# Optimization experiments

Measured on AMD Instinct MI355X. Metric: run time of the kernel, lower is better.

Reference implementation:

```python
import jax, jax.numpy as jnp
import numpy as np

D_MODEL = 1024
NUM_HEADS = 16
D_K = D_MODEL // NUM_HEADS
B, S = 4, 2048


def setup_inputs() -> dict:
    key = jax.random.key(0)
    k1, k2, k3 = jax.random.split(key, 3)
    x = jax.random.normal(k1, (B, S, D_MODEL), dtype=jnp.float32)
    w_qkv = jax.random.normal(k2, (3, NUM_HEADS, D_K, D_MODEL), dtype=jnp.float32) / np.sqrt(D_MODEL)
    w_o = jax.random.normal(k3, (D_MODEL, D_MODEL), dtype=jnp.float32) / np.sqrt(D_MODEL)
    return {"x": x, "w_qkv": w_qkv, "w_o": w_o}


def reference(x, w_qkv, w_o):
    # x: [b, s, m]; w_qkv: [3, h, k, m]; w_o: [m, m]
    seq_len = x.shape[-2]
    d_k = w_qkv.shape[-2]
    # fused QKV projection for all heads: [3, b, h, s, k]
    qkv = jnp.einsum('bsm,qhkm->qbhsk', x, w_qkv)
    Q, K, V = qkv[0], qkv[1], qkv[2]
    # attention scores [b, h, s, s]
    scores = jnp.einsum('bhsk,bhtk->bhst', Q, K) / jnp.sqrt(jnp.asarray(d_k, x.dtype))
    # causal mask: position t > s is masked
    causal = jnp.tril(jnp.ones((seq_len, seq_len), dtype=bool))
    scores = jnp.where(causal, scores, -jnp.inf)
    probs = jax.nn.softmax(scores, axis=-1)
    # attn_pdrop = 0.0 -> dropout is identity
    attn = jnp.einsum('bhst,bhtk->bhsk', probs, V)
    # concat heads: [b, s, h*k]
    b, h, s, k = attn.shape
    attn_cat = jnp.transpose(attn, (0, 2, 1, 3)).reshape(b, s, h * k)
    # output projection: y = attn_cat @ w_o^T
    return jnp.einsum('bsd,md->bsm', attn_cat, w_o)
```

## Files before the change

### kernel.cpp

```cpp
#include <hip/hip_runtime.h>
#include <hip/hip_bf16.h>


#define D_MODEL 1024
#define NUM_HEADS 16
#define D_KD 64
#define B_SZ 4
#define S_LEN 2048
#define ROWS (B_SZ * S_LEN)
#define QKV_N (3 * D_MODEL)

typedef __attribute__((ext_vector_type(8))) short short8;
typedef __attribute__((ext_vector_type(4))) float f32x4;
typedef __attribute__((ext_vector_type(16))) float f32x16;
typedef unsigned short ushort_t;

__device__ __forceinline__ unsigned f2bf(float f) {
    unsigned u = __builtin_bit_cast(unsigned, f);
    return (u + 0x7FFFu + ((u >> 16) & 1u)) >> 16;
}
__device__ __forceinline__ uint2 pack_bf16x4(float4 v) {
    uint2 u;
    u.x = f2bf(v.x) | (f2bf(v.y) << 16);
    u.y = f2bf(v.z) | (f2bf(v.w) << 16);
    return u;
}
__device__ __forceinline__ void gload16(void* lds, const void* g) {
    __builtin_amdgcn_global_load_lds(
        (const __attribute__((address_space(1))) unsigned int*)(g),
        (__attribute__((address_space(3))) unsigned int*)(lds), 16, 0, 0);
}

__global__ __launch_bounds__(256) void cvt_bf16(const float* __restrict__ src,
                                                ushort_t* __restrict__ dst, int n4) {
    int i = blockIdx.x * blockDim.x + threadIdx.x;
    const int stride = gridDim.x * blockDim.x;
    for (; i < n4; i += stride) {
        float4 v = reinterpret_cast<const float4*>(src)[i];
        *reinterpret_cast<uint2*>(&dst[(size_t)i * 4]) = pack_bf16x4(v);
    }
}

template <int MODE>
__global__ __launch_bounds__(256) void gemm_bt_bf16(const ushort_t* __restrict__ A,
                                                    const ushort_t* __restrict__ Bm,
                                                    ushort_t* __restrict__ Cb,
                                                    float* __restrict__ Cf,
                                                    int M, int N, int K) {
    __shared__ ushort_t As[128 * 32];
    __shared__ ushort_t Bs[128 * 32];

    const int t = threadIdx.x;
    const int lane = t & 63;
    const int w = t >> 6;
    const int wr = w >> 1, wc = w & 1;
    const int row0 = blockIdx.y * 128;
    const int col0 = blockIdx.x * 128;

    const int srow = t >> 2;
    const int sk8 = (t & 3) << 3;

    const ushort_t* Ag = A + (size_t)(row0 + srow) * K + sk8;
    const ushort_t* Bg = Bm + (size_t)(col0 + srow) * K + sk8;
    ushort_t* ldsA0 = &As[(size_t)t * 8];
    ushort_t* ldsA1 = &As[(size_t)(t + 256) * 8];
    ushort_t* ldsB0 = &Bs[(size_t)t * 8];
    ushort_t* ldsB1 = &Bs[(size_t)(t + 256) * 8];

    f32x4 acc[4][4];
#pragma unroll
    for (int m = 0; m < 4; ++m)
#pragma unroll
        for (int n = 0; n < 4; ++n)
#pragma unroll
            for (int j = 0; j < 4; ++j) acc[m][n][j] = 0.f;

    const int q8 = (lane >> 4) << 3;
    const int frA = wr * 64 + (lane & 15);
    const int frB = wc * 64 + (lane & 15);
    const int NT = K >> 5;

    for (int kt = 0; kt < NT; ++kt) {
        const int k0 = kt << 5;
        __syncthreads();
        gload16(ldsA0, Ag + k0);
        gload16(ldsA1, Ag + (size_t)64 * K + k0);
        gload16(ldsB0, Bg + k0);
        gload16(ldsB1, Bg + (size_t)64 * K + k0);
        __syncthreads();

        short8 afr[4], bfr[4];
#pragma unroll
        for (int m = 0; m < 4; ++m)
            afr[m] = *reinterpret_cast<const short8*>(&As[(frA + m * 16) * 32 + q8]);
#pragma unroll
        for (int n = 0; n < 4; ++n)
            bfr[n] = *reinterpret_cast<const short8*>(&Bs[(frB + n * 16) * 32 + q8]);
#pragma unroll
        for (int m = 0; m < 4; ++m)
#pragma unroll
            for (int n = 0; n < 4; ++n)
                acc[m][n] = __builtin_amdgcn_mfma_f32_16x16x32_bf16(afr[m], bfr[n],
                                                                    acc[m][n], 0, 0, 0);
    }

    const int orow = row0 + wr * 64 + ((lane >> 4) << 2);
    const int ocol = col0 + wc * 64 + (lane & 15);
#pragma unroll
    for (int m = 0; m < 4; ++m)
#pragma unroll
        for (int n = 0; n < 4; ++n) {
            const int cg = ocol + n * 16;
#pragma unroll
            for (int j = 0; j < 4; ++j) {
                const int rg = orow + m * 16 + j;
                float v = acc[m][n][j];
                if (MODE == 0) {
                    const int q = cg >> 10, hh = (cg >> 6) & 15, kk = cg & 63;
                    const int bb = rg >> 11, s = rg & 2047;
                    if (q == 0) v *= 0.125f;
                    Cb[((((size_t)q * B_SZ + bb) * NUM_HEADS + hh) * S_LEN + s) * D_KD + kk] =
                        (ushort_t)f2bf(v);
                } else {
                    Cf[(size_t)rg * N + cg] = v;
                }
            }
        }
}

__global__ __launch_bounds__(512, 2) void flash_attn_mfma_v3(const ushort_t* __restrict__ qkv,
                                                             ushort_t* __restrict__ attn_out) {
    const int qb = (int)gridDim.x - 1 - (int)blockIdx.x;
    const int h = blockIdx.y;
    const int b = blockIdx.z;
    const int t = threadIdx.x;
    const int lane = t & 63;
    const int w = t >> 6;
    const int l31 = lane & 31;
    const int hi = lane >> 5;

    __shared__ ushort_t smem[256 * 72];
    __shared__ float fbuf[8][32];
    ushort_t* Qs = smem;
    ushort_t* Ks = smem;
    ushort_t* Vt = smem + 64 * 72;

    const size_t head_elems = (size_t)S_LEN * D_KD;
    const ushort_t* Qg = qkv + (((size_t)0 * B_SZ + b) * NUM_HEADS + h) * head_elems;
    const ushort_t* Kg = qkv + (((size_t)1 * B_SZ + b) * NUM_HEADS + h) * head_elems;
    const ushort_t* Vg = qkv + (((size_t)2 * B_SZ + b) * NUM_HEADS + h) * head_elems;

    const int q0 = qb * 256;
    const int qmin = q0 + 32 * w;

#pragma unroll
    for (int lx = 0; lx < 4; ++lx) {
        int idx = t + lx * 512;
        int r = idx >> 3;
        int c8 = (idx & 7) << 3;
        *reinterpret_cast<uint4*>(&Qs[r * 72 + c8]) =
            *reinterpret_cast<const uint4*>(&Qg[(size_t)(q0 + r) * D_KD + c8]);
    }
    __syncthreads();

    short8 qfr[4];
#pragma unroll
    for (int ks = 0; ks < 4; ++ks)
        qfr[ks] = *reinterpret_cast<const short8*>(&Qs[(32 * w + l31) * 72 + 16 * ks + 8 * hi]);

    f32x16 oacc[2];
#pragma unroll
    for (int n = 0; n < 2; ++n)
#pragma unroll
        for (int j = 0; j < 16; ++j) oacc[n][j] = 0.f;
    float m = -1e30f, lsum = 0.f;

    const int nt = 4 * (qb + 1);
    for (int tt = 0; tt < nt; ++tt) {
        const int c0 = tt * 64;
        __syncthreads();

        if (w < 4) {
#pragma unroll
            for (int i = 0; i < 2; ++i) {
                int j = t + i * 256;
                int r = j >> 3;
                int c8 = (j & 7) << 3;
                *reinterpret_cast<uint4*>(&Ks[r * 72 + c8]) =
                    *reinterpret_cast<const uint4*>(&Kg[(size_t)(c0 + r) * D_KD + c8]);
            }
        } else {
            int t2 = t - 256;
            int tp = t2 & 31, dg = t2 >> 5;
            int t0 = tp * 2, d0 = dg * 8;
            uint4 va = *reinterpret_cast<const uint4*>(&Vg[(size_t)(c0 + t0) * D_KD + d0]);
            uint4 vb = *reinterpret_cast<const uint4*>(&Vg[(size_t)(c0 + t0 + 1) * D_KD + d0]);
            const ushort_t* ua = reinterpret_cast<const ushort_t*>(&va);
            const ushort_t* ub = reinterpret_cast<const ushort_t*>(&vb);
#pragma unroll
            for (int d = 0; d < 8; ++d) {
                unsigned u = (unsigned)ua[d] | ((unsigned)ub[d] << 16);
                *reinterpret_cast<unsigned*>(&Vt[(d0 + d) * 72 + t0]) = u;
            }
        }
        __syncthreads();

        for (int st = 0; st < 2; ++st) {
            const int t0s = c0 + 32 * st;
            if (t0s > qmin) break;
            const bool diag = (t0s == qmin);

            f32x16 s;
#pragma unroll
            for (int j = 0; j < 16; ++j) s[j] = 0.f;
            __builtin_amdgcn_s_setprio(1);
#pragma unroll
            for (int ks = 0; ks < 4; ++ks) {
                short8 ka = *reinterpret_cast<const short8*>(
                    &Ks[(32 * st + l31) * 72 + 16 * ks + 8 * hi]);
                s = __builtin_amdgcn_mfma_f32_32x32x16_bf16(ka, qfr[ks], s, 0, 0, 0);
            }
            __builtin_amdgcn_s_setprio(0);
            if (diag) {
#pragma unroll
                for (int reg = 0; reg < 16; ++reg) {
                    const int tloc = (reg & 3) + 8 * (reg >> 2) + 4 * hi;
                    if (tloc > l31) s[reg] = -1e30f;
                }
            }

            float pm = s[0];
#pragma unroll
            for (int reg = 1; reg < 16; ++reg) pm = fmaxf(pm, s[reg]);
            pm = fmaxf(pm, __shfl_xor(pm, 32));

            if (!__all(pm <= m + 8.0f)) {
                const float mnew = fmaxf(m, pm);
                const float al = __expf(m - mnew);
                m = mnew;
                lsum *= al;
                fbuf[w][l31] = al;
#pragma unroll
                for (int g = 0; g < 4; ++g) {
                    float4 a4 = *reinterpret_cast<float4*>(&fbuf[w][8 * g + 4 * hi]);
                    const float* ap = reinterpret_cast<const float*>(&a4);
#pragma unroll
                    for (int j = 0; j < 4; ++j) {
                        oacc[0][4 * g + j] *= ap[j];
                        oacc[1][4 * g + j] *= ap[j];
                    }
                }
            }

            float p[16];
            float ps = 0.f;
#pragma unroll
            for (int reg = 0; reg < 16; ++reg) {
                p[reg] = __expf(s[reg] - m);
                ps += p[reg];
            }
            ps += __shfl_xor(ps, 32);
            lsum += ps;

            unsigned pk[8], sw[8];
#pragma unroll
            for (int i = 0; i < 8; ++i) pk[i] = f2bf(p[2 * i]) | (f2bf(p[2 * i + 1]) << 16);
#pragma unroll
            for (int i = 0; i < 8; ++i) sw[i] = (unsigned)__shfl_xor((int)pk[i], 32);

            union { unsigned u[4]; short8 s8; } a0, a1;
            a0.u[0] = hi ? sw[2] : pk[0];
            a0.u[1] = hi ? sw[3] : pk[1];
            a0.u[2] = hi ? pk[2] : sw[0];
            a0.u[3] = hi ? pk[3] : sw[1];
            a1.u[0] = hi ? sw[6] : pk[4];
            a1.u[1] = hi ? sw[7] : pk[5];
            a1.u[2] = hi ? pk[6] : sw[4];
            a1.u[3] = hi ? pk[7] : sw[5];

            __builtin_amdgcn_s_setprio(1);
#pragma unroll
            for (int n = 0; n < 2; ++n) {
                const ushort_t* vrow = &Vt[(32 * n + l31) * 72 + 32 * st + 8 * hi];
                short8 vb0 = *reinterpret_cast<const short8*>(vrow);
                short8 vb1 = *reinterpret_cast<const short8*>(vrow + 16);
                oacc[n] = __builtin_amdgcn_mfma_f32_32x32x16_bf16(a0.s8, vb0, oacc[n], 0, 0, 0);
                oacc[n] = __builtin_amdgcn_mfma_f32_32x32x16_bf16(a1.s8, vb1, oacc[n], 0, 0, 0);
            }
            __builtin_amdgcn_s_setprio(0);
        }
    }

    const float inv = 1.f / lsum;
    fbuf[w][l31] = inv;
#pragma unroll
    for (int g = 0; g < 4; ++g) {
        float4 i4 = *reinterpret_cast<float4*>(&fbuf[w][8 * g + 4 * hi]);
        const float* ip = reinterpret_cast<const float*>(&i4);
#pragma unroll
        for (int j = 0; j < 4; ++j) {
            const int reg = 4 * g + j;
            const int qrow = q0 + 32 * w + 8 * g + 4 * hi + j;
            const size_t base = ((size_t)(b * S_LEN + qrow)) * D_MODEL + h * D_KD + l31;
            attn_out[base] = (ushort_t)f2bf(oacc[0][reg] * ip[j]);
            attn_out[base + 32] = (ushort_t)f2bf(oacc[1][reg] * ip[j]);
        }
    }
}

extern "C" void kernel_launch(void* const* d_in, const int* in_sizes, int n_in,
                              void* d_out, int out_size, void* d_ws, size_t ws_size,
                              hipStream_t stream) {
    const float* x = (const float*)d_in[0];
    const float* w_qkv = (const float*)d_in[1];
    const float* w_o = (const float*)d_in[2];
    float* out = (float*)d_out;

    ushort_t* xb = (ushort_t*)d_ws;
    ushort_t* wqb = xb + 8388608;
    ushort_t* wob = wqb + 3145728;
    ushort_t* qkvb = wob + 1048576;
    ushort_t* attnb = qkvb + 25165824;

    cvt_bf16<<<2048, 256, 0, stream>>>(x, xb, 8388608 / 4);
    cvt_bf16<<<1024, 256, 0, stream>>>(w_qkv, wqb, 3145728 / 4);
    cvt_bf16<<<512, 256, 0, stream>>>(w_o, wob, 1048576 / 4);

    gemm_bt_bf16<0><<<dim3(QKV_N / 128, ROWS / 128), dim3(256), 0, stream>>>(
        xb, wqb, qkvb, nullptr, ROWS, QKV_N, D_MODEL);
    flash_attn_mfma_v3<<<dim3(S_LEN / 256, NUM_HEADS, B_SZ), dim3(512), 0, stream>>>(qkvb, attnb);
    gemm_bt_bf16<1><<<dim3(D_MODEL / 128, ROWS / 128), dim3(256), 0, stream>>>(
        attnb, wob, nullptr, out, ROWS, D_MODEL, D_MODEL);
}
```

Measured before the change: 311.7 us.

## Deepen GEMM K-tile, swizzle workgroups, use exp2 softmax and builtin bf16 conversion

The GEMM now stages a 64-wide K slice per iteration, which halves the number of barrier-separated load/compute rounds, and remaps block indices with an XCD-style swizzle for better L2 locality. The attention softmax switches to base-2 exponentials by folding log2(e) into the Q scale, and the deferred-rescale threshold is raised to match. Hand-written round-to-nearest bf16 conversion is replaced by the __float2bfloat16 intrinsic. The larger LDS tiles raise LDS use per GEMM block, which may lower occupancy.

```diff
diff --git a/kernel.cpp b/kernel.cpp
--- a/kernel.cpp
+++ b/kernel.cpp
@@ -10,20 +10,19 @@
 #define ROWS (B_SZ * S_LEN)
 #define QKV_N (3 * D_MODEL)
 
+#define QSCALE 0.18033688f
+#define DEFER_THR 11.5415603f
+
 typedef __attribute__((ext_vector_type(8))) short short8;
 typedef __attribute__((ext_vector_type(4))) float f32x4;
 typedef __attribute__((ext_vector_type(16))) float f32x16;
 typedef unsigned short ushort_t;
 
-__device__ __forceinline__ unsigned f2bf(float f) {
-    unsigned u = __builtin_bit_cast(unsigned, f);
-    return (u + 0x7FFFu + ((u >> 16) & 1u)) >> 16;
-}
-__device__ __forceinline__ uint2 pack_bf16x4(float4 v) {
-    uint2 u;
-    u.x = f2bf(v.x) | (f2bf(v.y) << 16);
-    u.y = f2bf(v.z) | (f2bf(v.w) << 16);
-    return u;
+__device__ __forceinline__ ushort_t bf1(float a) {
+    return __builtin_bit_cast(unsigned short, __float2bfloat16(a));
+}
+__device__ __forceinline__ unsigned packbf2(float a, float b) {
+    return (unsigned)bf1(a) | ((unsigned)bf1(b) << 16);
 }
 __device__ __forceinline__ void gload16(void* lds, const void* g) {
     __builtin_amdgcn_global_load_lds(
@@ -37,7 +36,10 @@
     const int stride = gridDim.x * blockDim.x;
     for (; i < n4; i += stride) {
         float4 v = reinterpret_cast<const float4*>(src)[i];
-        *reinterpret_cast<uint2*>(&dst[(size_t)i * 4]) = pack_bf16x4(v);
+        uint2 u;
+        u.x = packbf2(v.x, v.y);
+        u.y = packbf2(v.z, v.w);
+        *reinterpret_cast<uint2*>(&dst[(size_t)i * 4]) = u;
     }
 }
 
@@ -47,25 +49,28 @@
                                                     ushort_t* __restrict__ Cb,
                                                     float* __restrict__ Cf,
                                                     int M, int N, int K) {
-    __shared__ ushort_t As[128 * 32];
-    __shared__ ushort_t Bs[128 * 32];
+    __shared__ ushort_t As[2 * 4096];
+    __shared__ ushort_t Bs[2 * 4096];
+
+    const int nwg = gridDim.x * gridDim.y;
+    const int orig = blockIdx.y * gridDim.x + blockIdx.x;
+    const int cpx = nwg >> 3;
+    const int swz = (orig & 7) * cpx + (orig >> 3);
+    const int bx = swz % gridDim.x;
+    const int by = swz / gridDim.x;
 
     const int t = threadIdx.x;
     const int lane = t & 63;
     const int w = t >> 6;
     const int wr = w >> 1, wc = w & 1;
-    const int row0 = blockIdx.y * 128;
-    const int col0 = blockIdx.x * 128;
+    const int row0 = by * 128;
+    const int col0 = bx * 128;
 
     const int srow = t >> 2;
     const int sk8 = (t & 3) << 3;
 
     const ushort_t* Ag = A + (size_t)(row0 + srow) * K + sk8;
     const ushort_t* Bg = Bm + (size_t)(col0 + srow) * K + sk8;
-    ushort_t* ldsA0 = &As[(size_t)t * 8];
-    ushort_t* ldsA1 = &As[(size_t)(t + 256) * 8];
-    ushort_t* ldsB0 = &Bs[(size_t)t * 8];
-    ushort_t* ldsB1 = &Bs[(size_t)(t + 256) * 8];
 
     f32x4 acc[4][4];
 #pragma unroll
@@ -78,30 +83,45 @@
     const int q8 = (lane >> 4) << 3;
     const int frA = wr * 64 + (lane & 15);
     const int frB = wc * 64 + (lane & 15);
-    const int NT = K >> 5;
+    const int NT = K >> 6;
 
     for (int kt = 0; kt < NT; ++kt) {
-        const int k0 = kt << 5;
+        const int k0 = kt << 6;
         __syncthreads();
-        gload16(ldsA0, Ag + k0);
-        gload16(ldsA1, Ag + (size_t)64 * K + k0);
-        gload16(ldsB0, Bg + k0);
-        gload16(ldsB1, Bg + (size_t)64 * K + k0);
+#pragma unroll
+        for (int kh = 0; kh < 2; ++kh) {
+            const int kw = k0 + kh * 32;
+#pragma unroll
+            for (int i2 = 0; i2 < 2; ++i2) {
+                ushort_t* dA = &As[kh * 4096 + (i2 * 256 + t) * 8];
+                ushort_t* dB = &Bs[kh * 4096 + (i2 * 256 + t) * 8];
+                gload16(dA, Ag + (size_t)i2 * 64 * K + kw);
+                gload16(dB, Bg + (size_t)i2 * 64 * K + kw);
+            }
+        }
         __syncthreads();
 
-        short8 afr[4], bfr[4];
+        short8 afr[4][2], bfr[4][2];
 #pragma unroll
         for (int m = 0; m < 4; ++m)
-            afr[m] = *reinterpret_cast<const short8*>(&As[(frA + m * 16) * 32 + q8]);
+#pragma unroll
+            for (int kh = 0; kh < 2; ++kh)
+                afr[m][kh] = *reinterpret_cast<const short8*>(
+                    &As[kh * 4096 + (frA + m * 16) * 32 + q8]);
 #pragma unroll
         for (int n = 0; n < 4; ++n)
-            bfr[n] = *reinterpret_cast<const short8*>(&Bs[(frB + n * 16) * 32 + q8]);
-#pragma unroll
-        for (int m = 0; m < 4; ++m)
-#pragma unroll
-            for (int n = 0; n < 4; ++n)
-                acc[m][n] = __builtin_amdgcn_mfma_f32_16x16x32_bf16(afr[m], bfr[n],
-                                                                    acc[m][n], 0, 0, 0);
+#pragma unroll
+            for (int kh = 0; kh < 2; ++kh)
+                bfr[n][kh] = *reinterpret_cast<const short8*>(
+                    &Bs[kh * 4096 + (frB + n * 16) * 32 + q8]);
+#pragma unroll
+        for (int kh = 0; kh < 2; ++kh)
+#pragma unroll
+            for (int m = 0; m < 4; ++m)
+#pragma unroll
+                for (int n = 0; n < 4; ++n)
+                    acc[m][n] = __builtin_amdgcn_mfma_f32_16x16x32_bf16(
+                        afr[m][kh], bfr[n][kh], acc[m][n], 0, 0, 0);
     }
 
     const int orow = row0 + wr * 64 + ((lane >> 4) << 2);
@@ -118,9 +138,9 @@
                 if (MODE == 0) {
                     const int q = cg >> 10, hh = (cg >> 6) & 15, kk = cg & 63;
                     const int bb = rg >> 11, s = rg & 2047;
-                    if (q == 0) v *= 0.125f;
+                    if (q == 0) v *= QSCALE;
                     Cb[((((size_t)q * B_SZ + bb) * NUM_HEADS + hh) * S_LEN + s) * D_KD + kk] =
-                        (ushort_t)f2bf(v);
+                        bf1(v);
                 } else {
                     Cf[(size_t)rg * N + cg] = v;
                 }
@@ -128,7 +148,7 @@
         }
 }
 
-__global__ __launch_bounds__(512, 2) void flash_attn_mfma_v3(const ushort_t* __restrict__ qkv,
+__global__ __launch_bounds__(512, 2) void flash_attn_mfma_v5(const ushort_t* __restrict__ qkv,
                                                              ushort_t* __restrict__ attn_out) {
     const int qb = (int)gridDim.x - 1 - (int)blockIdx.x;
     const int h = blockIdx.y;
@@ -152,6 +172,7 @@
 
     const int q0 = qb * 256;
     const int qmin = q0 + 32 * w;
+    const int nt = 4 * (qb + 1);
 
 #pragma unroll
     for (int lx = 0; lx < 4; ++lx) {
@@ -175,7 +196,6 @@
         for (int j = 0; j < 16; ++j) oacc[n][j] = 0.f;
     float m = -1e30f, lsum = 0.f;
 
-    const int nt = 4 * (qb + 1);
     for (int tt = 0; tt < nt; ++tt) {
         const int c0 = tt * 64;
         __syncthreads();
@@ -234,9 +254,9 @@
             for (int reg = 1; reg < 16; ++reg) pm = fmaxf(pm, s[reg]);
             pm = fmaxf(pm, __shfl_xor(pm, 32));
 
-            if (!__all(pm <= m + 8.0f)) {
+            if (!__all(pm <= m + DEFER_THR)) {
                 const float mnew = fmaxf(m, pm);
-                const float al = __expf(m - mnew);
+                const float al = exp2f(m - mnew);
                 m = mnew;
                 lsum *= al;
                 fbuf[w][l31] = al;
@@ -256,7 +276,7 @@
             float ps = 0.f;
 #pragma unroll
             for (int reg = 0; reg < 16; ++reg) {
-                p[reg] = __expf(s[reg] - m);
+                p[reg] = exp2f(s[reg] - m);
                 ps += p[reg];
             }
             ps += __shfl_xor(ps, 32);
@@ -264,7 +284,7 @@
 
             unsigned pk[8], sw[8];
 #pragma unroll
-            for (int i = 0; i < 8; ++i) pk[i] = f2bf(p[2 * i]) | (f2bf(p[2 * i + 1]) << 16);
+            for (int i = 0; i < 8; ++i) pk[i] = packbf2(p[2 * i], p[2 * i + 1]);
 #pragma unroll
             for (int i = 0; i < 8; ++i) sw[i] = (unsigned)__shfl_xor((int)pk[i], 32);
 
@@ -302,8 +322,8 @@
             const int reg = 4 * g + j;
             const int qrow = q0 + 32 * w + 8 * g + 4 * hi + j;
             const size_t base = ((size_t)(b * S_LEN + qrow)) * D_MODEL + h * D_KD + l31;
-            attn_out[base] = (ushort_t)f2bf(oacc[0][reg] * ip[j]);
-            attn_out[base + 32] = (ushort_t)f2bf(oacc[1][reg] * ip[j]);
+            attn_out[base] = bf1(oacc[0][reg] * ip[j]);
+            attn_out[base + 32] = bf1(oacc[1][reg] * ip[j]);
         }
     }
 }
@@ -328,7 +348,7 @@
 
     gemm_bt_bf16<0><<<dim3(QKV_N / 128, ROWS / 128), dim3(256), 0, stream>>>(
         xb, wqb, qkvb, nullptr, ROWS, QKV_N, D_MODEL);
-    flash_attn_mfma_v3<<<dim3(S_LEN / 256, NUM_HEADS, B_SZ), dim3(512), 0, stream>>>(qkvb, attnb);
+    flash_attn_mfma_v5<<<dim3(S_LEN / 256, NUM_HEADS, B_SZ), dim3(512), 0, stream>>>(qkvb, attnb);
     gemm_bt_bf16<1><<<dim3(D_MODEL / 128, ROWS / 128), dim3(256), 0, stream>>>(
         attnb, wob, nullptr, out, ROWS, D_MODEL, D_MODEL);
 }
```

New measurement: 323.7 us. +3.9%, slower.
